# Optimization experiments

Measured on AMD Instinct MI355X. Metric: run time of the kernel, lower is better.

Reference implementation:

```python
import jax, jax.numpy as jnp
import numpy as np

N_NODES = 100000
N_EDGES = 3200000
FEAT = 16


def gcn_conv(x, src, dst, W, b):
    # PyG GCNConv: add self-loops, symmetric normalization deg^{-1/2}(A+I)deg^{-1/2},
    # then linear transform and scatter-add aggregation.
    n = x.shape[0]
    loop = jnp.arange(n, dtype=src.dtype)
    s = jnp.concatenate([src, loop])
    d = jnp.concatenate([dst, loop])
    deg = jax.ops.segment_sum(jnp.ones_like(d, dtype=x.dtype), d, num_segments=n)
    dinv = jnp.where(deg > 0, jax.lax.rsqrt(deg), 0.0)
    norm = dinv[s] * dinv[d]  # [E+N]
    h = x @ W  # [N, out]
    msg = h[s] * norm[:, None]  # gather + weight
    out = jax.ops.segment_sum(msg, d, num_segments=n)  # scatter-add
    return out + b


def setup_inputs() -> dict:
    key = jax.random.key(0)
    k1, k2, k3, k4 = jax.random.split(key, 4)
    scale = 1.0 / np.sqrt(FEAT)
    return {
        "x": jax.random.normal(k1, (N_NODES, FEAT), dtype=jnp.float32),
        "edge_index": jax.random.randint(k2, (2, N_EDGES), 0, N_NODES, dtype=jnp.int64) if jax.config.jax_enable_x64 else jax.random.randint(k2, (2, N_EDGES), 0, N_NODES, dtype=jnp.int32),
        "W1": jax.random.normal(k3, (FEAT, 16), dtype=jnp.float32) * scale,
        "b1": jnp.zeros((16,), dtype=jnp.float32),
        "W2": jax.random.normal(k4, (16, FEAT), dtype=jnp.float32) * scale,
        "b2": jnp.zeros((FEAT,), dtype=jnp.float32),
    }


def reference(x, edge_index, W1, b1, W2, b2):
    src, dst = edge_index[0], edge_index[1]
    h = gcn_conv(x, src, dst, W1, b1)
    h = jax.nn.relu(h)
    out = gcn_conv(h, src, dst, W2, b2)
    return out
```

## Files before the change

kernel.cpp:

```cpp
#include <hip/hip_runtime.h>

#define F 16
#define BSHIFT 8
#define NPB 256
#define NB 391
#define CH 4096
#define BCAP 9216

typedef float f4 __attribute__((ext_vector_type(4)));


__global__ void init_cursor_kernel(unsigned* __restrict__ cursor) {
    int i = threadIdx.x;
    if (i < NB) cursor[i * 16] = (unsigned)(i * BCAP);
}

__global__ __launch_bounds__(512) void
reorder_kernel(const int* __restrict__ src, const int* __restrict__ dst,
               unsigned* __restrict__ cursor, unsigned* __restrict__ recs, int E) {
    __shared__ unsigned lsorted[CH];
    __shared__ unsigned short lbkt[CH];
    __shared__ unsigned cnt[NB];
    __shared__ unsigned lstart[NB + 1];
    int t = threadIdx.x, b = blockIdx.x;
    int e0 = b * CH;
    int cnt_e = E - e0; if (cnt_e > CH) cnt_e = CH;

    for (int i = t; i < NB; i += 512) cnt[i] = 0;
    __syncthreads();
    unsigned pk[8], rs[8];
#pragma unroll
    for (int j = 0; j < 8; ++j) {
        int i = t + j * 512;
        pk[j] = 0xFFFFFFFFu;
        if (i < cnt_e) {
            unsigned d = (unsigned)dst[e0 + i];
            rs[j] = (unsigned)src[e0 + i];
            unsigned bk = d >> BSHIFT;
            unsigned r = atomicAdd(&cnt[bk], 1u);
            pk[j] = bk | ((d & 255u) << 9) | (r << 17);
        }
    }
    __syncthreads();
    if (t < 64) {
        unsigned run = 0;
        for (int c = 0; c < NB; c += 64) {
            int idx = c + t;
            unsigned v = (idx < NB) ? cnt[idx] : 0u;
            unsigned inc = v;
#pragma unroll
            for (int d = 1; d < 64; d <<= 1) {
                unsigned o = __shfl_up(inc, d, 64);
                if (t >= d) inc += o;
            }
            if (idx < NB) lstart[idx] = run + inc - v;
            run += __shfl(inc, 63, 64);
        }
        if (t == 0) lstart[NB] = (unsigned)cnt_e;
    }
    __syncthreads();
    {
        int s0 = (int)(((unsigned)b * 101u) % (unsigned)NB);
        for (int q = t; q < NB; q += 512) {
            int i = s0 + q; if (i >= NB) i -= NB;
            unsigned c = cnt[i];
            if (c) cnt[i] = atomicAdd(&cursor[i * 16], c);
        }
    }
    __syncthreads();
#pragma unroll
    for (int j = 0; j < 8; ++j) {
        int i = t + j * 512;
        if (i < cnt_e) {
            unsigned p = pk[j];
            unsigned bk = p & 0x1FFu;
            unsigned pos = lstart[bk] + (p >> 17);
            lsorted[pos] = rs[j] | (((p >> 9) & 255u) << 17);
            lbkt[pos] = (unsigned short)bk;
        }
    }
    __syncthreads();
    for (int i = t; i < cnt_e; i += 512) {
        unsigned bk = lbkt[i];
        recs[cnt[bk] + ((unsigned)i - lstart[bk])] = lsorted[i];
    }
}

__global__ __launch_bounds__(1024) void
sort2_kernel(const unsigned* __restrict__ recs, const unsigned* __restrict__ cursor,
             unsigned* __restrict__ srcs, int* __restrict__ noff, int* __restrict__ nend,
             float* __restrict__ dinv, const float* __restrict__ x,
             float* __restrict__ z, int n) {
    __shared__ unsigned lsort[BCAP];
    __shared__ unsigned cnt[NPB];
    __shared__ unsigned ex[NPB];
    __shared__ float ldv[NPB];
    __shared__ unsigned wtot[4];
    int t = threadIdx.x, b = blockIdx.x;
    int e0 = b * BCAP;
    int used = (int)(cursor[b * 16] - (unsigned)e0);
    if (t < NPB) cnt[t] = 0;
    __syncthreads();
    unsigned pk[9], rsr[9];
#pragma unroll
    for (int j = 0; j < 9; ++j) {
        int i = t + j * 1024;
        pk[j] = 0xFFFFFFFFu;
        if (i < used) {
            unsigned rec = recs[e0 + i];
            unsigned node = rec >> 17;
            rsr[j] = rec & 0x1FFFFu;
            unsigned r = atomicAdd(&cnt[node], 1u);
            pk[j] = node | (r << 8);
        }
    }
    __syncthreads();
    if (t < NPB) {
        unsigned c = cnt[t];
        unsigned inc = c;
        int lane = t & 63, w = t >> 6;
#pragma unroll
        for (int d = 1; d < 64; d <<= 1) {
            unsigned o = __shfl_up(inc, d, 64);
            if (lane >= d) inc += o;
        }
        if (lane == 63) wtot[w] = inc;
        __syncthreads();
        unsigned wbase = 0;
        for (int i = 0; i < w; ++i) wbase += wtot[i];
        unsigned e = wbase + inc - c;
        ex[t] = e;
        float dv = rsqrtf((float)c + 1.0f);
        ldv[t] = dv;
        int node = b * NPB + t;
        if (node < n) {
            noff[node] = e0 + (int)e;
            nend[node] = e0 + (int)(e + c);
            dinv[node] = dv;
        }
    } else {
        __syncthreads();
    }
    __syncthreads();
#pragma unroll
    for (int j = 0; j < 9; ++j) {
        int i = t + j * 1024;
        if (i < used) {
            unsigned p = pk[j];
            lsort[ex[p & 255u] + (p >> 8)] = rsr[j];
        }
    }
    __syncthreads();
    for (int i = t; i < used; i += 1024) srcs[e0 + i] = lsort[i];
    {
        int node = b * NPB + (t >> 2);
        if (node < n) {
            f4 v = ((const f4*)x)[(size_t)b * 1024 + t];
            float dv = ldv[t >> 2];
            v *= dv;
            ((f4*)z)[(size_t)b * 1024 + t] = v;
        }
    }
}

__global__ void agg_csr_kernel(const float* __restrict__ hin, const unsigned* __restrict__ srcs,
                               const int* __restrict__ noff, const int* __restrict__ nend,
                               const float* __restrict__ dinv,
                               const float* __restrict__ W, const float* __restrict__ bias,
                               float* __restrict__ outp, int n, int mode) {
    __shared__ float a1[64][F + 1];
    __shared__ float Ws[F * F];
    int t = threadIdx.x;
    int g = t >> 2, c = t & 3;
    Ws[t] = W[t];
    int node = blockIdx.x * 64 + g;
    const f4* h4 = (const f4*)hin;
    float di = 0.f;
    if (node < n) {
        di = dinv[node];
        int e0 = noff[node], e1 = nend[node];
        f4 s0 = {0,0,0,0}, s1 = {0,0,0,0}, s2 = {0,0,0,0}, s3 = {0,0,0,0};
        int e = e0;
        for (; e + 4 <= e1; e += 4) {
            int ia = srcs[e], ib = srcs[e + 1], ic = srcs[e + 2], id = srcs[e + 3];
            f4 va = __builtin_nontemporal_load(&h4[(size_t)ia * 4 + c]);
            f4 vb = __builtin_nontemporal_load(&h4[(size_t)ib * 4 + c]);
            f4 vc = __builtin_nontemporal_load(&h4[(size_t)ic * 4 + c]);
            f4 vd = __builtin_nontemporal_load(&h4[(size_t)id * 4 + c]);
            s0 += va; s1 += vb; s2 += vc; s3 += vd;
        }
        for (; e < e1; ++e) {
            f4 va = __builtin_nontemporal_load(&h4[(size_t)srcs[e] * 4 + c]);
            s0 += va;
        }
        f4 self = h4[(size_t)node * 4 + c];
        f4 s = (s0 + s1) + (s2 + s3) + self;
        a1[g][c * 4 + 0] = s[0];
        a1[g][c * 4 + 1] = s[1];
        a1[g][c * 4 + 2] = s[2];
        a1[g][c * 4 + 3] = s[3];
    }
    __syncthreads();
    if (node < n) {
        float ox = 0.f, oy = 0.f, oz = 0.f, ow = 0.f;
        int j = c * 4;
#pragma unroll
        for (int k = 0; k < F; ++k) {
            float ak = a1[g][k];
            ox += ak * Ws[k * F + j + 0];
            oy += ak * Ws[k * F + j + 1];
            oz += ak * Ws[k * F + j + 2];
            ow += ak * Ws[k * F + j + 3];
        }
        const f4 bi = ((const f4*)bias)[c];
        ox = di * ox + bi[0]; oy = di * oy + bi[1];
        oz = di * oz + bi[2]; ow = di * ow + bi[3];
        if (mode == 1) {
            ox = fmaxf(ox, 0.f) * di; oy = fmaxf(oy, 0.f) * di;
            oz = fmaxf(oz, 0.f) * di; ow = fmaxf(ow, 0.f) * di;
        }
        f4 o = {ox, oy, oz, ow};
        ((f4*)outp)[(size_t)node * 4 + c] = o;
    }
}


__global__ void deg_kernel(const int* __restrict__ dst, float* __restrict__ deg, int E) {
    int e = blockIdx.x * blockDim.x + threadIdx.x;
    if (e < E) atomicAdd(&deg[dst[e]], 1.0f);
}
__global__ void dinv_kernel(float* __restrict__ deg, int n) {
    int i = blockIdx.x * blockDim.x + threadIdx.x;
    if (i < n) deg[i] = rsqrtf(deg[i] + 1.0f);
}
__global__ void linear2_kernel(const float* __restrict__ in, const float* __restrict__ acc,
                               const float* __restrict__ dinv, const float* __restrict__ W,
                               const float* __restrict__ bias, float* __restrict__ out,
                               int n, int mode) {
    __shared__ float Ws[F * F];
    __shared__ float As[16][F + 1];
    int t = threadIdx.x;
    Ws[t] = W[t];
    int nb = t >> 4, j = t & 15;
    int i = blockIdx.x * 16 + nb;
    float di = 0.f, v = 0.f;
    if (i < n) {
        di = dinv[i]; v = in[i * F + j];
        if (mode) { v = di * (acc[i * F + j] + v) + bias[j]; v = fmaxf(v, 0.f); }
    }
    As[nb][j] = v;
    __syncthreads();
    if (i < n) {
        float s = 0.f;
#pragma unroll
        for (int k = 0; k < F; ++k) s += As[nb][k] * Ws[k * F + j];
        out[i * F + j] = s * di;
    }
}
__global__ void scatter_kernel(const int* __restrict__ src, const int* __restrict__ dst,
                               const float* __restrict__ h, float* __restrict__ acc, int E) {
    int t = blockIdx.x * blockDim.x + threadIdx.x;
    int e = t >> 4, j = t & 15;
    if (e < E) atomicAdd(&acc[dst[e] * F + j], h[src[e] * F + j]);
}
__global__ void out_kernel(const float* __restrict__ acc, const float* __restrict__ h,
                           const float* __restrict__ dinv, const float* __restrict__ bias,
                           float* __restrict__ out, int n) {
    int t = blockIdx.x * blockDim.x + threadIdx.x;
    if (t < n * F) {
        int i = t >> 4, j = t & 15;
        out[t] = dinv[i] * (acc[t] + h[t]) + bias[j];
    }
}


extern "C" void kernel_launch(void* const* d_in, const int* in_sizes, int n_in,
                              void* d_out, int out_size, void* d_ws, size_t ws_size,
                              hipStream_t stream) {
    const float* x  = (const float*)d_in[0];
    const int*   ei = (const int*)d_in[1];
    const float* W1 = (const float*)d_in[2];
    const float* b1 = (const float*)d_in[3];
    const float* W2 = (const float*)d_in[4];
    const float* b2 = (const float*)d_in[5];
    float* outp = (float*)d_out;

    const int N = in_sizes[0] / F;
    const int E = in_sizes[1] / 2;
    const int* src = ei;
    const int* dst = ei + E;

    const int nb_rt = (N + NPB - 1) >> BSHIFT;
    const size_t RC = (size_t)NB * BCAP;
    size_t need = sizeof(unsigned) * ((size_t)N * 19 + 2 * RC + 16 * NB);

    if (nb_rt == NB && E <= CH * 65535 && ws_size >= need) {
        float* dinv = (float*)d_ws;
        float* z = dinv + N;
        unsigned* recs = (unsigned*)(z + (size_t)F * N);
        float* y = (float*)recs;
        unsigned* srcs = recs + RC;
        int* noff = (int*)(srcs + RC);
        int* nend = noff + N;
        unsigned* cursor = (unsigned*)(nend + N);

        init_cursor_kernel<<<1, 512, 0, stream>>>(cursor);
        reorder_kernel<<<(E + CH - 1) / CH, 512, 0, stream>>>(src, dst, cursor, recs, E);
        sort2_kernel<<<NB, 1024, 0, stream>>>(recs, cursor, srcs, noff, nend, dinv, x, z, N);
        agg_csr_kernel<<<(N + 63) / 64, 256, 0, stream>>>(z, srcs, noff, nend, dinv, W1, b1, y, N, 1);
        agg_csr_kernel<<<(N + 63) / 64, 256, 0, stream>>>(y, srcs, noff, nend, dinv, W2, b2, outp, N, 2);
    } else {
        float* dinv = (float*)d_ws;
        float* h = dinv + N;
        float* acc = h + (size_t)F * N;
        hipMemsetAsync(dinv, 0, (size_t)N * sizeof(float), stream);
        hipMemsetAsync(acc, 0, (size_t)F * N * sizeof(float), stream);
        deg_kernel<<<(E + 255) / 256, 256, 0, stream>>>(dst, dinv, E);
        dinv_kernel<<<(N + 255) / 256, 256, 0, stream>>>(dinv, N);
        linear2_kernel<<<(N + 15) / 16, 256, 0, stream>>>(x, nullptr, dinv, W1, nullptr, h, N, 0);
        scatter_kernel<<<((size_t)E * F + 255) / 256, 256, 0, stream>>>(src, dst, h, acc, E);
        linear2_kernel<<<(N + 15) / 16, 256, 0, stream>>>(h, acc, dinv, W2, b1, h, N, 1);
        hipMemsetAsync(acc, 0, (size_t)F * N * sizeof(float), stream);
        scatter_kernel<<<((size_t)E * F + 255) / 256, 256, 0, stream>>>(src, dst, h, acc, E);
        out_kernel<<<((size_t)N * F + 255) / 256, 256, 0, stream>>>(acc, h, dinv, b2, outp, N);
    }
}
```

Baseline: 238.9 us.

## Fuse first-layer aggregation into sort kernel using global degree atomics

Degrees are now counted with global atomics in the reorder pass, and a new small kernel computes dinv and the prescaled features z before the sort. Because z is ready at that point, the per-bucket sort kernel can aggregate layer 1 straight from its shared-memory sorted sources and apply W1/ReLU, which removes one full CSR aggregation launch and its reread of the source indices. This adds 3.2M global atomics, a memset and an extra launch. Nontemporal loads are also replaced with normal cached loads in the remaining aggregation.

```diff
diff --git a/kernel.cpp b/kernel.cpp
--- a/kernel.cpp
+++ b/kernel.cpp
@@ -17,7 +17,8 @@
 
 __global__ __launch_bounds__(512) void
 reorder_kernel(const int* __restrict__ src, const int* __restrict__ dst,
-               unsigned* __restrict__ cursor, unsigned* __restrict__ recs, int E) {
+               unsigned* __restrict__ cursor, unsigned* __restrict__ recs,
+               unsigned* __restrict__ deg, int E) {
     __shared__ unsigned lsorted[CH];
     __shared__ unsigned short lbkt[CH];
     __shared__ unsigned cnt[NB];
@@ -38,6 +39,7 @@
             rs[j] = (unsigned)src[e0 + i];
             unsigned bk = d >> BSHIFT;
             unsigned r = atomicAdd(&cnt[bk], 1u);
+            atomicAdd(&deg[d], 1u);
             pk[j] = bk | ((d & 255u) << 9) | (r << 17);
         }
     }
@@ -86,12 +88,27 @@
     }
 }
 
-__global__ __launch_bounds__(1024) void
-sort2_kernel(const unsigned* __restrict__ recs, const unsigned* __restrict__ cursor,
-             unsigned* __restrict__ srcs, int* __restrict__ noff, int* __restrict__ nend,
-             float* __restrict__ dinv, const float* __restrict__ x,
-             float* __restrict__ z, int n) {
+__global__ void dinvz_kernel(const unsigned* __restrict__ deg, float* __restrict__ dinv,
+                             const float* __restrict__ x, float* __restrict__ z, int n) {
+    int i = blockIdx.x * 256 + threadIdx.x;
+    int node = i >> 2;
+    if (node < n) {
+        float dv = rsqrtf((float)deg[node] + 1.0f);
+        if ((i & 3) == 0) dinv[node] = dv;
+        f4 v = ((const f4*)x)[i];
+        v *= dv;
+        ((f4*)z)[i] = v;
+    }
+}
+
+__global__ __launch_bounds__(1024, 2) void
+sort2agg_kernel(const unsigned* __restrict__ recs, const unsigned* __restrict__ cursor,
+                unsigned* __restrict__ srcs, int* __restrict__ noff, int* __restrict__ nend,
+                const float* __restrict__ z, const float* __restrict__ W,
+                const float* __restrict__ bias, float* __restrict__ y, int n) {
     __shared__ unsigned lsort[BCAP];
+    __shared__ float a1[NPB][F + 1];
+    __shared__ float Ws[F * F];
     __shared__ unsigned cnt[NPB];
     __shared__ unsigned ex[NPB];
     __shared__ float ldv[NPB];
@@ -100,6 +117,7 @@
     int e0 = b * BCAP;
     int used = (int)(cursor[b * 16] - (unsigned)e0);
     if (t < NPB) cnt[t] = 0;
+    if (t < 256) Ws[t] = W[t];
     __syncthreads();
     unsigned pk[9], rsr[9];
 #pragma unroll
@@ -130,13 +148,11 @@
         for (int i = 0; i < w; ++i) wbase += wtot[i];
         unsigned e = wbase + inc - c;
         ex[t] = e;
-        float dv = rsqrtf((float)c + 1.0f);
-        ldv[t] = dv;
+        ldv[t] = rsqrtf((float)c + 1.0f);
         int node = b * NPB + t;
         if (node < n) {
             noff[node] = e0 + (int)e;
             nend[node] = e0 + (int)(e + c);
-            dinv[node] = dv;
         }
     } else {
         __syncthreads();
@@ -153,12 +169,49 @@
     __syncthreads();
     for (int i = t; i < used; i += 1024) srcs[e0 + i] = lsort[i];
     {
-        int node = b * NPB + (t >> 2);
+        int g = t >> 2, c = t & 3;
+        int node = b * NPB + g;
+        const f4* h4 = (const f4*)z;
         if (node < n) {
-            f4 v = ((const f4*)x)[(size_t)b * 1024 + t];
-            float dv = ldv[t >> 2];
-            v *= dv;
-            ((f4*)z)[(size_t)b * 1024 + t] = v;
+            int el = (int)ex[g], eh = el + (int)cnt[g];
+            f4 s0 = {0,0,0,0}, s1 = {0,0,0,0}, s2 = {0,0,0,0}, s3 = {0,0,0,0};
+            int e = el;
+            for (; e + 4 <= eh; e += 4) {
+                int ia = lsort[e], ib = lsort[e + 1], ic = lsort[e + 2], id = lsort[e + 3];
+                f4 va = h4[(size_t)ia * 4 + c];
+                f4 vb = h4[(size_t)ib * 4 + c];
+                f4 vc = h4[(size_t)ic * 4 + c];
+                f4 vd = h4[(size_t)id * 4 + c];
+                s0 += va; s1 += vb; s2 += vc; s3 += vd;
+            }
+            for (; e < eh; ++e) s0 += h4[(size_t)lsort[e] * 4 + c];
+            f4 self = h4[(size_t)node * 4 + c];
+            f4 s = (s0 + s1) + (s2 + s3) + self;
+            a1[g][c * 4 + 0] = s[0];
+            a1[g][c * 4 + 1] = s[1];
+            a1[g][c * 4 + 2] = s[2];
+            a1[g][c * 4 + 3] = s[3];
+        }
+        __syncthreads();
+        if (node < n) {
+            float di = ldv[g];
+            float ox = 0.f, oy = 0.f, oz = 0.f, ow = 0.f;
+            int j = c * 4;
+#pragma unroll
+            for (int k = 0; k < F; ++k) {
+                float ak = a1[g][k];
+                ox += ak * Ws[k * F + j + 0];
+                oy += ak * Ws[k * F + j + 1];
+                oz += ak * Ws[k * F + j + 2];
+                ow += ak * Ws[k * F + j + 3];
+            }
+            const f4 bi = ((const f4*)bias)[c];
+            ox = fmaxf(di * ox + bi[0], 0.f) * di;
+            oy = fmaxf(di * oy + bi[1], 0.f) * di;
+            oz = fmaxf(di * oz + bi[2], 0.f) * di;
+            ow = fmaxf(di * ow + bi[3], 0.f) * di;
+            f4 o = {ox, oy, oz, ow};
+            ((f4*)y)[(size_t)node * 4 + c] = o;
         }
     }
 }
@@ -167,7 +220,7 @@
                                const int* __restrict__ noff, const int* __restrict__ nend,
                                const float* __restrict__ dinv,
                                const float* __restrict__ W, const float* __restrict__ bias,
-                               float* __restrict__ outp, int n, int mode) {
+                               float* __restrict__ outp, int n) {
     __shared__ float a1[64][F + 1];
     __shared__ float Ws[F * F];
     int t = threadIdx.x;
@@ -183,16 +236,13 @@
         int e = e0;
         for (; e + 4 <= e1; e += 4) {
             int ia = srcs[e], ib = srcs[e + 1], ic = srcs[e + 2], id = srcs[e + 3];
-            f4 va = __builtin_nontemporal_load(&h4[(size_t)ia * 4 + c]);
-            f4 vb = __builtin_nontemporal_load(&h4[(size_t)ib * 4 + c]);
-            f4 vc = __builtin_nontemporal_load(&h4[(size_t)ic * 4 + c]);
-            f4 vd = __builtin_nontemporal_load(&h4[(size_t)id * 4 + c]);
+            f4 va = h4[(size_t)ia * 4 + c];
+            f4 vb = h4[(size_t)ib * 4 + c];
+            f4 vc = h4[(size_t)ic * 4 + c];
+            f4 vd = h4[(size_t)id * 4 + c];
             s0 += va; s1 += vb; s2 += vc; s3 += vd;
         }
-        for (; e < e1; ++e) {
-            f4 va = __builtin_nontemporal_load(&h4[(size_t)srcs[e] * 4 + c]);
-            s0 += va;
-        }
+        for (; e < e1; ++e) s0 += h4[(size_t)srcs[e] * 4 + c];
         f4 self = h4[(size_t)node * 4 + c];
         f4 s = (s0 + s1) + (s2 + s3) + self;
         a1[g][c * 4 + 0] = s[0];
@@ -213,13 +263,7 @@
             ow += ak * Ws[k * F + j + 3];
         }
         const f4 bi = ((const f4*)bias)[c];
-        ox = di * ox + bi[0]; oy = di * oy + bi[1];
-        oz = di * oz + bi[2]; ow = di * ow + bi[3];
-        if (mode == 1) {
-            ox = fmaxf(ox, 0.f) * di; oy = fmaxf(oy, 0.f) * di;
-            oz = fmaxf(oz, 0.f) * di; ow = fmaxf(ow, 0.f) * di;
-        }
-        f4 o = {ox, oy, oz, ow};
+        f4 o = {di * ox + bi[0], di * oy + bi[1], di * oz + bi[2], di * ow + bi[3]};
         ((f4*)outp)[(size_t)node * 4 + c] = o;
     }
 }
@@ -292,23 +336,25 @@
 
     const int nb_rt = (N + NPB - 1) >> BSHIFT;
     const size_t RC = (size_t)NB * BCAP;
-    size_t need = sizeof(unsigned) * ((size_t)N * 19 + 2 * RC + 16 * NB);
+    size_t need = sizeof(unsigned) * ((size_t)N * 36 + 2 * RC + 16 * NB);
 
     if (nb_rt == NB && E <= CH * 65535 && ws_size >= need) {
         float* dinv = (float*)d_ws;
-        float* z = dinv + N;
-        unsigned* recs = (unsigned*)(z + (size_t)F * N);
-        float* y = (float*)recs;
+        unsigned* deg = (unsigned*)(dinv + N);
+        float* z = (float*)(deg + N);
+        float* y = z + (size_t)F * N;
+        unsigned* recs = (unsigned*)(y + (size_t)F * N);
         unsigned* srcs = recs + RC;
         int* noff = (int*)(srcs + RC);
         int* nend = noff + N;
         unsigned* cursor = (unsigned*)(nend + N);
 
+        hipMemsetAsync(deg, 0, (size_t)N * sizeof(unsigned), stream);
         init_cursor_kernel<<<1, 512, 0, stream>>>(cursor);
-        reorder_kernel<<<(E + CH - 1) / CH, 512, 0, stream>>>(src, dst, cursor, recs, E);
-        sort2_kernel<<<NB, 1024, 0, stream>>>(recs, cursor, srcs, noff, nend, dinv, x, z, N);
-        agg_csr_kernel<<<(N + 63) / 64, 256, 0, stream>>>(z, srcs, noff, nend, dinv, W1, b1, y, N, 1);
-        agg_csr_kernel<<<(N + 63) / 64, 256, 0, stream>>>(y, srcs, noff, nend, dinv, W2, b2, outp, N, 2);
+        reorder_kernel<<<(E + CH - 1) / CH, 512, 0, stream>>>(src, dst, cursor, recs, deg, E);
+        dinvz_kernel<<<((N * 4) + 255) / 256, 256, 0, stream>>>(deg, dinv, x, z, N);
+        sort2agg_kernel<<<NB, 1024, 0, stream>>>(recs, cursor, srcs, noff, nend, z, W1, b1, y, N);
+        agg_csr_kernel<<<(N + 63) / 64, 256, 0, stream>>>(y, srcs, noff, nend, dinv, W2, b2, outp, N);
     } else {
         float* dinv = (float*)d_ws;
         float* h = dinv + N;
```

After: 319.3 us. 33.7% more time.
